# Kernel tuning notes

Measured on AMD Instinct MI355X. Metric: run time of the kernel, lower is better.

## Reference

```python
import jax, jax.numpy as jnp
import numpy as np

HEADS = 16
HEAD_DIM = 64  # embed_size 1024 // 16


def setup_inputs() -> dict:
    key = jax.random.key(0)
    ks = jax.random.split(key, 6)
    N, S, E = 2, 2048, 1024
    return {
        "values": jax.random.normal(ks[0], (N, S, E), dtype=jnp.float32),
        "keys": jax.random.normal(ks[1], (N, S, E), dtype=jnp.float32),
        "queries": jax.random.normal(ks[2], (N, S, E), dtype=jnp.float32),
        "Wv": jax.random.normal(ks[3], (E, E), dtype=jnp.float32) * (E ** -0.5),
        "Wk": jax.random.normal(ks[4], (E, E), dtype=jnp.float32) * (E ** -0.5),
        "Wq": jax.random.normal(ks[5], (E, E), dtype=jnp.float32) * (E ** -0.5),
    }


def reference(values, keys, queries, Wv, Wk, Wq):
    N, Sq, E = queries.shape
    Sk = keys.shape[1]
    H, D = HEADS, HEAD_DIM
    # linear projections (torch Linear: x @ W^T), then split heads
    v = (values @ Wv.T).reshape(N, Sk, H, D)
    k = (keys @ Wk.T).reshape(N, Sk, H, D)
    q = (queries @ Wq.T).reshape(N, Sq, H, D)
    # QK^T -> [N, H, Q, K]
    scores = jnp.einsum("nqhd,nkhd->nhqk", q, k)
    # no mask (original forward takes mask=None path); scale by sqrt(head_dim)
    attn = jax.nn.softmax(scores / jnp.asarray(D, scores.dtype) ** 0.5, axis=-1)
    # AV -> [N, Q, H, D] -> [N, Q, E]; note: fc_out is never applied in the original forward
    out = jnp.einsum("nhql,nlhd->nqhd", attn, v).reshape(N, Sq, H * D)
    return out
```

## Files before the change

### kernel.cpp

```cpp
#include <hip/hip_runtime.h>
#include <math.h>

#define SEQ 2048
#define EMB 1024
#define NH  16
#define HD  64

typedef __attribute__((ext_vector_type(8))) short short8;
typedef __attribute__((ext_vector_type(4))) float f32x4;

static const size_t XE = (size_t)2 * SEQ * EMB;
static const size_t WE = (size_t)EMB * EMB;

static __device__ __forceinline__ short f2bf(float f) {
    unsigned u = __builtin_bit_cast(unsigned, f);
    u = u + 0x7fffu + ((u >> 16) & 1u);
    return (short)(u >> 16);
}

#if __has_builtin(__builtin_amdgcn_cvt_pk_bf16_f32)
typedef __attribute__((ext_vector_type(2))) __bf16 bf16x2;
static __device__ __forceinline__ unsigned pk2(float a, float b) {
    bf16x2 v = __builtin_amdgcn_cvt_pk_bf16_f32(a, b);
    return __builtin_bit_cast(unsigned, v);
}
#else
static __device__ __forceinline__ unsigned pk2(float a, float b) {
    return (unsigned)(unsigned short)f2bf(a) |
           ((unsigned)(unsigned short)f2bf(b) << 16);
}
#endif

static __device__ __forceinline__ short8 cvt8(float4 a, float4 b) {
    union { unsigned u[4]; short8 s; } r;
    r.u[0] = pk2(a.x, a.y); r.u[1] = pk2(a.z, a.w);
    r.u[2] = pk2(b.x, b.y); r.u[3] = pk2(b.z, b.w);
    return r.s;
}

static __device__ __forceinline__ void gload16(const void* g, void* l) {
    __builtin_amdgcn_global_load_lds(
        (const __attribute__((address_space(1))) void*)g,
        (__attribute__((address_space(3))) void*)l, 16, 0, 0);
}

__global__ __launch_bounds__(256)
void cvt_w(const float* __restrict__ s0, const float* __restrict__ s1,
           const float* __restrict__ s2, short* __restrict__ d) {
    int id = blockIdx.x;
    int seg = id >> 9, off = id & 511;
    const float* s = (seg == 0) ? s0 : (seg == 1) ? s1 : s2;
    short* dd = d + (size_t)seg * WE;
    size_t i = (size_t)off * 256 + threadIdx.x;
    const float4* sp = (const float4*)s;
    float4 a = sp[2 * i], b = sp[2 * i + 1];
    *(short8*)(dd + i * 8) = cvt8(a, b);
}

#define ES_STRIDE 136
__global__ __launch_bounds__(256, 3)
void proj(const float* __restrict__ Xq, const float* __restrict__ Xk,
          const float* __restrict__ Xv, const short* __restrict__ Wb,
          short* __restrict__ qb, short* __restrict__ kbuf,
          short* __restrict__ vt) {
    __shared__ __align__(16) char lds_raw[49152];
    float4* Fs = (float4*)lds_raw;
    short8* Hs = (short8*)(lds_raw + 32768);
    short*  Es = (short*)lds_raw;

    const int L = blockIdx.x;
    const int xcd = L & 7, i = L >> 3;
    const int z = i >> 5;
    const int m = i & 31;
    const int ty = xcd * 4 + (m & 3);
    const int tx = m >> 2;

    const float* Fop; const short* Hop; short* C;
    if (z == 0)      { Fop = Xq; Hop = Wb;           C = qb;   }
    else if (z == 1) { Fop = Xk; Hop = Wb + WE;      C = kbuf; }
    else             { Fop = Xv; Hop = Wb + 2 * WE;  C = vt;   }
    const int fr0 = ty * 128;
    const int hr0 = tx * 128;

    const int t = threadIdx.x, w = t >> 6, lane = t & 63;
    const int l15 = lane & 15, quad = lane >> 4;
    const int mh = (w >> 1) * 64, nh2 = (w & 1) * 64;

    auto stageF = [&](int p, int k0) {
#pragma unroll
        for (int j = 0; j < 4; ++j) {
            int g = j * 256 + t, row = g >> 3, c = g & 7;
            int cs = c ^ (row & 7);
            gload16(Fop + (size_t)(fr0 + row) * EMB + k0 + cs * 4,
                    &Fs[p * 1024 + j * 256 + w * 64]);
        }
    };
    auto stageH = [&](int p, int k0) {
#pragma unroll
        for (int j = 0; j < 2; ++j) {
            int g = j * 256 + t, row = g & 127, c = g >> 7;
            gload16(Hop + (size_t)(hr0 + row) * EMB + k0 + c * 8,
                    &Hs[p * 512 + j * 256 + w * 64]);
        }
    };
    auto fragF = [&](int p, int fr) -> short8 {
        int r7 = fr & 7;
        float4 a = Fs[p * 1024 + fr * 8 + ((2 * quad) ^ r7)];
        float4 b = Fs[p * 1024 + fr * 8 + ((2 * quad + 1) ^ r7)];
        return cvt8(a, b);
    };

    f32x4 acc[4][4];
#pragma unroll
    for (int a = 0; a < 4; ++a)
#pragma unroll
        for (int b = 0; b < 4; ++b) acc[a][b] = 0.f;

    stageF(0, 0);
    stageH(0, 0);

    int p = 0;
    for (int k0 = 0; k0 < EMB; k0 += 32, p ^= 1) {
        __syncthreads();
        if (k0 + 32 < EMB) { stageF(p ^ 1, k0 + 32); stageH(p ^ 1, k0 + 32); }

        short8 af[4], bf[4];
        if (z < 2) {
#pragma unroll
            for (int mi = 0; mi < 4; ++mi)
                af[mi] = fragF(p, mh + mi * 16 + l15);
#pragma unroll
            for (int ni = 0; ni < 4; ++ni)
                bf[ni] = Hs[p * 512 + quad * 128 + nh2 + ni * 16 + l15];
        } else {
#pragma unroll
            for (int mi = 0; mi < 4; ++mi)
                af[mi] = Hs[p * 512 + quad * 128 + mh + mi * 16 + l15];
#pragma unroll
            for (int ni = 0; ni < 4; ++ni)
                bf[ni] = fragF(p, nh2 + ni * 16 + l15);
        }
#pragma unroll
        for (int mi = 0; mi < 4; ++mi)
#pragma unroll
            for (int ni = 0; ni < 4; ++ni)
                acc[mi][ni] = __builtin_amdgcn_mfma_f32_16x16x32_bf16(
                    af[mi], bf[ni], acc[mi][ni], 0, 0, 0);
    }

    __syncthreads();
#pragma unroll
    for (int mi = 0; mi < 4; ++mi)
#pragma unroll
        for (int ni = 0; ni < 4; ++ni)
#pragma unroll
            for (int r = 0; r < 4; ++r) {
                int lr_ = mh + mi * 16 + quad * 4 + r;
                int lc_ = nh2 + ni * 16 + l15;
                Es[lr_ * ES_STRIDE + lc_] = f2bf(acc[mi][ni][r]);
            }
    __syncthreads();
    {
        int row = t >> 1, half = t & 1;
        const short* src = Es + row * ES_STRIDE + half * 64;
        short* dst;
        if (z < 2) {
            dst = C + (size_t)(fr0 + row) * EMB + hr0 + half * 64;
        } else {
            int bz = fr0 >> 11, s0 = fr0 & 2047;
            dst = C + ((size_t)bz * EMB + hr0 + row) * SEQ + s0 + half * 64;
        }
#pragma unroll
        for (int j = 0; j < 8; ++j)
            *(short8*)(dst + j * 8) = *(const short8*)(src + j * 8);
    }
}

__global__ __launch_bounds__(256, 2)
void attn_mfma(const short* __restrict__ Qg, const short* __restrict__ Kg,
               const short* __restrict__ Vtg, float* __restrict__ OutD) {
    __shared__ short8 QPs[1024];
    __shared__ short8 Ks[2][1024];
    __shared__ short8 Vs[2][1024];

    const int t = threadIdx.x, w = t >> 6, lane = t & 63;
    const int l15 = lane & 15, quad = lane >> 4;
    const int lr3 = lane >> 3, lc7 = lane & 7;
    const int L = blockIdx.x;
    const int xcd = L & 7, i = L >> 3;
    const int bh = xcd * 4 + (i & 3);
    const int q0 = (i >> 2) * 128;
    const int b = bh >> 4, h = bh & 15;
    const short* Qb = Qg + (size_t)b * SEQ * EMB + h * HD;
    const short* Kb = Kg + (size_t)b * SEQ * EMB + h * HD;
    const short* Vb = Vtg + ((size_t)b * EMB + h * HD) * SEQ;

    auto stageKV = [&](int p, int kt) {
#pragma unroll
        for (int j = 0; j < 4; ++j) {
            int rb = w * 32 + j * 8;
            int krow = rb + lr3;
            gload16(Kb + (size_t)(kt + krow) * EMB + ((lc7 ^ (krow & 7)) * 8),
                    &Ks[p][rb * 8]);
            int half = w >> 1, db = (w & 1) * 32 + j * 8;
            int d = db + lr3;
            gload16(Vb + (size_t)d * SEQ + kt + half * 64 + ((lc7 ^ (d & 7)) * 8),
                    &Vs[p][half * 512 + db * 8]);
        }
    };

#pragma unroll
    for (int j = 0; j < 4; ++j) {
        int rb = w * 32 + j * 8;
        int row = rb + lr3;
        gload16(Qb + (size_t)(q0 + row) * EMB + ((lc7 ^ (row & 7)) * 8),
                &QPs[rb * 8]);
    }
    stageKV(0, 0);
    __syncthreads();

    short8 qf[2][2];
#pragma unroll
    for (int qi = 0; qi < 2; ++qi)
#pragma unroll
        for (int kb2 = 0; kb2 < 2; ++kb2) {
            int row = w * 32 + qi * 16 + l15;
            qf[qi][kb2] = QPs[row * 8 + ((kb2 * 4 + quad) ^ (l15 & 7))];
        }

    f32x4 o[2][4];
    float lr[2] = {0.f, 0.f};
#pragma unroll
    for (int qi = 0; qi < 2; ++qi)
#pragma unroll
        for (int ni = 0; ni < 4; ++ni) o[qi][ni] = 0.f;
    const float cl2 = 0.18033688011112042f;
    const float c0  = 11.541560327111707f;

    int p = 0;
    for (int kt = 0; kt < SEQ; kt += 128, p ^= 1) {
        if (kt) __syncthreads();
        if (kt + 128 < SEQ) stageKV(p ^ 1, kt + 128);

#pragma unroll
        for (int half = 0; half < 2; ++half) {
            f32x4 s[4][2];
#pragma unroll
            for (int kblk = 0; kblk < 4; ++kblk)
#pragma unroll
                for (int qi = 0; qi < 2; ++qi) s[kblk][qi] = 0.f;
#pragma unroll
            for (int kb2 = 0; kb2 < 2; ++kb2) {
                short8 ak[4];
#pragma unroll
                for (int kblk = 0; kblk < 4; ++kblk) {
                    int row = half * 64 + kblk * 16 + l15;
                    ak[kblk] = Ks[p][row * 8 + ((kb2 * 4 + quad) ^ (l15 & 7))];
                }
#pragma unroll
                for (int kblk = 0; kblk < 4; ++kblk)
#pragma unroll
                    for (int qi = 0; qi < 2; ++qi)
                        s[kblk][qi] = __builtin_amdgcn_mfma_f32_16x16x32_bf16(
                            ak[kblk], qf[qi][kb2], s[kblk][qi], 0, 0, 0);
            }

#pragma unroll
            for (int qi = 0; qi < 2; ++qi) {
                int row = w * 32 + qi * 16 + l15;
#pragma unroll
                for (int kblk = 0; kblk < 4; ++kblk) {
                    float p0 = __builtin_amdgcn_exp2f(fmaf(s[kblk][qi][0], cl2, -c0));
                    float p1 = __builtin_amdgcn_exp2f(fmaf(s[kblk][qi][1], cl2, -c0));
                    float p2 = __builtin_amdgcn_exp2f(fmaf(s[kblk][qi][2], cl2, -c0));
                    float p3 = __builtin_amdgcn_exp2f(fmaf(s[kblk][qi][3], cl2, -c0));
                    lr[qi] += (p0 + p1) + (p2 + p3);
                    uint2 pv; pv.x = pk2(p0, p1); pv.y = pk2(p2, p3);
                    int kc = kblk * 2 + (quad >> 1);
                    *(uint2*)((char*)QPs +
                        (((row * 8 + (kc ^ (l15 & 7))) << 4) | ((quad & 1) << 3)))
                        = pv;
                }
            }

#pragma unroll
            for (int kb2 = 0; kb2 < 2; ++kb2) {
                short8 ap[2], bv[4];
#pragma unroll
                for (int qi = 0; qi < 2; ++qi) {
                    int row = w * 32 + qi * 16 + l15;
                    ap[qi] = QPs[row * 8 + ((kb2 * 4 + quad) ^ (l15 & 7))];
                }
#pragma unroll
                for (int ni = 0; ni < 4; ++ni) {
                    int dr = ni * 16 + l15;
                    bv[ni] = Vs[p][half * 512 + dr * 8 +
                                   ((kb2 * 4 + quad) ^ (l15 & 7))];
                }
#pragma unroll
                for (int qi = 0; qi < 2; ++qi)
#pragma unroll
                    for (int ni = 0; ni < 4; ++ni)
                        o[qi][ni] = __builtin_amdgcn_mfma_f32_16x16x32_bf16(
                            ap[qi], bv[ni], o[qi][ni], 0, 0, 0);
            }
        }
    }

#pragma unroll
    for (int qi = 0; qi < 2; ++qi) {
        float l = lr[qi];
        l += __shfl_xor(l, 16);
        l += __shfl_xor(l, 32);
        lr[qi] = l;
    }
#pragma unroll
    for (int qi = 0; qi < 2; ++qi)
#pragma unroll
        for (int r = 0; r < 4; ++r) {
            float inv = 1.0f / __shfl(lr[qi], quad * 4 + r);
            int q = q0 + w * 32 + qi * 16 + quad * 4 + r;
            float* op = OutD + ((size_t)b * SEQ + q) * EMB + h * HD;
#pragma unroll
            for (int ni = 0; ni < 4; ++ni)
                op[ni * 16 + l15] = o[qi][ni][r] * inv;
        }
}

extern "C" void kernel_launch(void* const* d_in, const int* in_sizes, int n_in,
                              void* d_out, int out_size, void* d_ws, size_t ws_size,
                              hipStream_t stream) {
    const float* values  = (const float*)d_in[0];
    const float* keys    = (const float*)d_in[1];
    const float* queries = (const float*)d_in[2];
    const float* Wv      = (const float*)d_in[3];
    const float* Wk      = (const float*)d_in[4];
    const float* Wq      = (const float*)d_in[5];
    float* out = (float*)d_out;

    short* qb = (short*)d_ws;
    short* kb = qb + XE;
    short* vt = kb + XE;
    short* wb = vt + XE;

    cvt_w<<<1536, 256, 0, stream>>>(Wq, Wk, Wv, wb);
    proj<<<768, 256, 0, stream>>>(queries, keys, values, wb, qb, kb, vt);
    attn_mfma<<<512, 256, 0, stream>>>(qb, kb, vt, out);
}
```

Baseline: 209.9 us.

## Pre-convert activations to bf16 in a separate pass before projection GEMM

The fp32-to-bf16 conversion of the input activations moves out of the projection GEMM's inner loop and into a standalone conversion kernel that also handles the weights. The projection then stages bf16 tiles straight from global memory, which shrinks its LDS footprint and lets the launch bound rise from 3 to 4 blocks per CU. In exchange there is an extra round trip through global memory: the fp32 inputs are read once and written back as bf16, then read again by the projection. Extra workspace is also needed for the converted activations.

```diff
diff --git a/kernel.cpp b/kernel.cpp
--- a/kernel.cpp
+++ b/kernel.cpp
@@ -45,27 +45,39 @@
 }
 
 __global__ __launch_bounds__(256)
-void cvt_w(const float* __restrict__ s0, const float* __restrict__ s1,
-           const float* __restrict__ s2, short* __restrict__ d) {
+void cvt_all(const float* __restrict__ xq, const float* __restrict__ xk,
+             const float* __restrict__ xv, const float* __restrict__ wq,
+             const float* __restrict__ wk, const float* __restrict__ wv,
+             short* __restrict__ dxq, short* __restrict__ dxk,
+             short* __restrict__ dxv, short* __restrict__ dw) {
     int id = blockIdx.x;
-    int seg = id >> 9, off = id & 511;
-    const float* s = (seg == 0) ? s0 : (seg == 1) ? s1 : s2;
-    short* dd = d + (size_t)seg * WE;
-    size_t i = (size_t)off * 256 + threadIdx.x;
+    const float* s; short* d; size_t i;
+    if (id < 6144) {
+        int seg = id >> 11, o = id & 2047;
+        s = (seg == 0) ? xq : (seg == 1) ? xk : xv;
+        d = (seg == 0) ? dxq : (seg == 1) ? dxk : dxv;
+        i = (size_t)o * 256 + threadIdx.x;
+    } else {
+        int wid = id - 6144;
+        int seg = wid >> 9, o = wid & 511;
+        s = (seg == 0) ? wq : (seg == 1) ? wk : wv;
+        d = dw + (size_t)seg * WE;
+        i = (size_t)o * 256 + threadIdx.x;
+    }
     const float4* sp = (const float4*)s;
     float4 a = sp[2 * i], b = sp[2 * i + 1];
-    *(short8*)(dd + i * 8) = cvt8(a, b);
+    *(short8*)(d + i * 8) = cvt8(a, b);
 }
 
 #define ES_STRIDE 136
-__global__ __launch_bounds__(256, 3)
-void proj(const float* __restrict__ Xq, const float* __restrict__ Xk,
-          const float* __restrict__ Xv, const short* __restrict__ Wb,
+__global__ __launch_bounds__(256, 4)
+void proj(const short* __restrict__ Xq, const short* __restrict__ Xk,
+          const short* __restrict__ Xv, const short* __restrict__ Wb,
           short* __restrict__ qb, short* __restrict__ kbuf,
           short* __restrict__ vt) {
-    __shared__ __align__(16) char lds_raw[49152];
-    float4* Fs = (float4*)lds_raw;
-    short8* Hs = (short8*)(lds_raw + 32768);
+    __shared__ __align__(16) char lds_raw[34816];
+    short8* Fs = (short8*)lds_raw;
+    short8* Hs = (short8*)(lds_raw + 16384);
     short*  Es = (short*)lds_raw;
 
     const int L = blockIdx.x;
@@ -75,7 +87,7 @@
     const int ty = xcd * 4 + (m & 3);
     const int tx = m >> 2;
 
-    const float* Fop; const short* Hop; short* C;
+    const short* Fop; const short* Hop; short* C;
     if (z == 0)      { Fop = Xq; Hop = Wb;           C = qb;   }
     else if (z == 1) { Fop = Xk; Hop = Wb + WE;      C = kbuf; }
     else             { Fop = Xv; Hop = Wb + 2 * WE;  C = vt;   }
@@ -86,28 +98,21 @@
     const int l15 = lane & 15, quad = lane >> 4;
     const int mh = (w >> 1) * 64, nh2 = (w & 1) * 64;
 
-    auto stageF = [&](int p, int k0) {
-#pragma unroll
-        for (int j = 0; j < 4; ++j) {
-            int g = j * 256 + t, row = g >> 3, c = g & 7;
-            int cs = c ^ (row & 7);
-            gload16(Fop + (size_t)(fr0 + row) * EMB + k0 + cs * 4,
-                    &Fs[p * 1024 + j * 256 + w * 64]);
+    auto stageF = [&](int pp, int k0) {
+#pragma unroll
+        for (int j = 0; j < 2; ++j) {
+            int g = j * 256 + t, row = g & 127, c = g >> 7;
+            gload16(Fop + (size_t)(fr0 + row) * EMB + k0 + c * 8,
+                    &Fs[pp * 512 + j * 256 + w * 64]);
         }
     };
-    auto stageH = [&](int p, int k0) {
+    auto stageH = [&](int pp, int k0) {
 #pragma unroll
         for (int j = 0; j < 2; ++j) {
             int g = j * 256 + t, row = g & 127, c = g >> 7;
             gload16(Hop + (size_t)(hr0 + row) * EMB + k0 + c * 8,
-                    &Hs[p * 512 + j * 256 + w * 64]);
-        }
-    };
-    auto fragF = [&](int p, int fr) -> short8 {
-        int r7 = fr & 7;
-        float4 a = Fs[p * 1024 + fr * 8 + ((2 * quad) ^ r7)];
-        float4 b = Fs[p * 1024 + fr * 8 + ((2 * quad + 1) ^ r7)];
-        return cvt8(a, b);
+                    &Hs[pp * 512 + j * 256 + w * 64]);
+        }
     };
 
     f32x4 acc[4][4];
@@ -128,7 +133,7 @@
         if (z < 2) {
 #pragma unroll
             for (int mi = 0; mi < 4; ++mi)
-                af[mi] = fragF(p, mh + mi * 16 + l15);
+                af[mi] = Fs[p * 512 + quad * 128 + mh + mi * 16 + l15];
 #pragma unroll
             for (int ni = 0; ni < 4; ++ni)
                 bf[ni] = Hs[p * 512 + quad * 128 + nh2 + ni * 16 + l15];
@@ -138,7 +143,7 @@
                 af[mi] = Hs[p * 512 + quad * 128 + mh + mi * 16 + l15];
 #pragma unroll
             for (int ni = 0; ni < 4; ++ni)
-                bf[ni] = fragF(p, nh2 + ni * 16 + l15);
+                bf[ni] = Fs[p * 512 + quad * 128 + nh2 + ni * 16 + l15];
         }
 #pragma unroll
         for (int mi = 0; mi < 4; ++mi)
@@ -338,12 +343,16 @@
     const float* Wq      = (const float*)d_in[5];
     float* out = (float*)d_out;
 
-    short* qb = (short*)d_ws;
-    short* kb = qb + XE;
-    short* vt = kb + XE;
-    short* wb = vt + XE;
-
-    cvt_w<<<1536, 256, 0, stream>>>(Wq, Wk, Wv, wb);
-    proj<<<768, 256, 0, stream>>>(queries, keys, values, wb, qb, kb, vt);
+    short* qb  = (short*)d_ws;
+    short* kb  = qb + XE;
+    short* vt  = kb + XE;
+    short* wb  = vt + XE;
+    short* xqb = wb + 3 * WE;
+    short* xkb = xqb + XE;
+    short* xvb = xkb + XE;
+
+    cvt_all<<<7680, 256, 0, stream>>>(queries, keys, values, Wq, Wk, Wv,
+                                      xqb, xkb, xvb, wb);
+    proj<<<768, 256, 0, stream>>>(xqb, xkb, xvb, wb, qb, kb, vt);
     attn_mfma<<<512, 256, 0, stream>>>(qb, kb, vt, out);
 }
```

New measurement: 214.2 us. 1.02x slower.
